# Performance work log

Measured on AMD Instinct MI355X. Metric: run time of the kernel, lower is better.

The kernel has to match this reference:

```python
import jax, jax.numpy as jnp
import numpy as np

S = 7          # side
B = 2          # boxes per cell
C = 20         # classes
L = S * S      # grid cells
NOOBJ = 0.5 * 1.0
OBJ   = 0.5 * 1.0
CLS   = 0.5 * 1.0
COORD = 0.5 * 5.0


def setup_inputs() -> dict:
    key = jax.random.key(0)
    k1, k2, k3 = jax.random.split(key, 3)
    n = 16384
    preds = jax.random.uniform(k1, (n, L * (C + 5 * B)), dtype=jnp.float32)
    labels = jax.random.uniform(k2, (n, L * (1 + C + 4)), dtype=jnp.float32)
    lab = labels.reshape(n, L, 1 + C + 4)
    obj_flag = (jax.random.uniform(k3, (n, L)) < 0.15).astype(jnp.float32)
    lab = lab.at[:, :, 0].set(obj_flag)
    labels = lab.reshape(n, -1)
    return {"preds": preds, "labels": labels}


def _iou(t, o):
    # t, o: [..., 4] boxes in (cx, cy, w, h); returns [...]
    left   = jnp.maximum(t[..., 0] - 0.5 * t[..., 2], o[..., 0] - 0.5 * o[..., 2])
    right  = jnp.minimum(t[..., 0] + 0.5 * t[..., 2], o[..., 0] + 0.5 * o[..., 2])
    top    = jnp.maximum(t[..., 1] - 0.5 * t[..., 3], o[..., 1] - 0.5 * o[..., 3])
    bottom = jnp.minimum(t[..., 1] + 0.5 * t[..., 3], o[..., 1] + 0.5 * o[..., 3])
    w = right - left
    h = bottom - top
    invalid = (w < 0) | (h < 0)
    inter = jnp.where(invalid, 0.0, w * h)
    union = t[..., 2] * t[..., 3] + o[..., 2] * o[..., 3] - inter
    return jnp.where(invalid, 0.0, inter / jnp.maximum(union, 1e-12))


def reference(preds, labels):
    n = preds.shape[0]
    pcls  = preds[:, : L * C].reshape(n, L, C)                       # [n,L,C]
    pconf = preds[:, L * C : L * C + L * B].reshape(n, L, B)          # [n,L,B]
    pbox  = preds[:, L * C + L * B :].reshape(n, L, B, 4)             # [n,L,B,4]

    lab  = labels.reshape(n, L, 1 + C + 4)
    obj  = lab[:, :, 0] != 0                                          # [n,L]
    tcls = lab[:, :, 1 : 1 + C]                                       # [n,L,C]
    tbox = lab[:, :, 1 + C :]                                         # [n,L,4] raw

    # --- best-box selection (on detached predictions, like .detach() in torch) ---
    o_raw = jax.lax.stop_gradient(pbox)
    o = jnp.concatenate([o_raw[..., :2] / S, o_raw[..., 2:] ** 2], axis=-1)      # [n,L,B,4]
    t = jnp.concatenate([tbox[..., :2] / S, tbox[..., 2:]], axis=-1)[:, :, None] # [n,L,1,4]
    t = jax.lax.stop_gradient(t)

    iou  = _iou(t, o)                                                 # [n,L,B]
    rmse = jnp.sqrt(jnp.sum((t - o) ** 2, axis=-1))                   # [n,L,B]
    max_iou = jnp.max(iou, axis=-1)
    # if any IoU>0 pick first argmax of IoU, else first argmin of RMSE (best_rmse init 20)
    best = jnp.where(max_iou > 0, jnp.argmax(iou, axis=-1), jnp.argmin(rmse, axis=-1))  # [n,L]
    best_iou = jnp.take_along_axis(iou, best[:, :, None], axis=-1)[..., 0]        # [n,L]

    onehot = jnp.arange(B) == best[:, :, None]                        # [n,L,B]
    mask_best = obj[:, :, None] & onehot

    # confidence delta: noobject everywhere, overwritten at best box of object cells
    conf_delta = jnp.where(mask_best,
                           OBJ * (best_iou[:, :, None] - pconf) ** 2,
                           NOOBJ * pconf ** 2)

    # class delta (object cells only)
    cls_delta = jnp.where(obj[:, :, None], CLS * (tcls - pcls) ** 2, 0.0)

    # coord delta at best box: raw truth x,y and sqrt(truth w,h) vs raw preds
    pbest = jnp.take_along_axis(pbox, best[:, :, None, None], axis=2)[:, :, 0]    # [n,L,4]
    ttarget = jnp.concatenate([tbox[..., :2], jnp.sqrt(tbox[..., 2:])], axis=-1)  # [n,L,4]
    coord_delta = jnp.where(obj[:, :, None], COORD * (ttarget - pbest) ** 2, 0.0)

    return jnp.nansum(conf_delta) + jnp.nansum(cls_delta) + jnp.nansum(coord_delta)
```

## Files before the change

kernel.cpp:

```cpp
#include <hip/hip_runtime.h>


#define L_CELLS 49
#define PRED_ROW 1470
#define LAB_ROW 1225
#define CONF_BASE 980
#define BOX_BASE 1078
#define W_NOOBJ 0.5f
#define W_OBJ 0.5f
#define W_CLS 0.5f
#define W_COORD 2.5f
#define INV_S (1.0f / 7.0f)

__global__ void zero_out_kernel(float* out) { out[0] = 0.0f; }

__global__ __launch_bounds__(256) void yolo_loss_kernel(
    const float* __restrict__ preds, const float* __restrict__ labels,
    float* __restrict__ out, int n) {
  int cell = blockIdx.x * blockDim.x + threadIdx.x;
  int total = n * L_CELLS;
  float acc = 0.0f;
  if (cell < total) {
    int sample = cell / L_CELLS;
    int l = cell - sample * L_CELLS;
    const float* rp = preds + (size_t)sample * PRED_ROW;
    const float* labc = labels + (size_t)sample * LAB_ROW + l * 25;

    float objf = labc[0];
    const float* confp = rp + CONF_BASE + l * 2;
    float c0 = confp[0];
    float c1 = confp[1];

    if (objf != 0.0f) {
      const float* boxp = rp + BOX_BASE + l * 8;
      float bx[8];
#pragma unroll
      for (int k = 0; k < 8; ++k) bx[k] = boxp[k];

      float tx = labc[21], ty = labc[22], tw = labc[23], th = labc[24];
      float t0 = tx * INV_S, t1 = ty * INV_S, t2 = tw, t3 = th;

      float iou[2], rmse2[2];
#pragma unroll
      for (int b = 0; b < 2; ++b) {
        float o0 = bx[4 * b + 0] * INV_S;
        float o1 = bx[4 * b + 1] * INV_S;
        float o2 = bx[4 * b + 2] * bx[4 * b + 2];
        float o3 = bx[4 * b + 3] * bx[4 * b + 3];
        float left = fmaxf(t0 - 0.5f * t2, o0 - 0.5f * o2);
        float right = fminf(t0 + 0.5f * t2, o0 + 0.5f * o2);
        float top = fmaxf(t1 - 0.5f * t3, o1 - 0.5f * o3);
        float bot = fminf(t1 + 0.5f * t3, o1 + 0.5f * o3);
        float w = right - left;
        float h = bot - top;
        bool invalid = (w < 0.0f) || (h < 0.0f);
        float inter = invalid ? 0.0f : w * h;
        float uni = t2 * t3 + o2 * o3 - inter;
        iou[b] = invalid ? 0.0f : inter / fmaxf(uni, 1e-12f);
        float d0 = t0 - o0, d1 = t1 - o1, d2 = t2 - o2, d3 = t3 - o3;
        rmse2[b] = d0 * d0 + d1 * d1 + d2 * d2 + d3 * d3;
      }

      float max_iou = fmaxf(iou[0], iou[1]);
      int best;
      if (max_iou > 0.0f)
        best = (iou[1] > iou[0]) ? 1 : 0;
      else
        best = (rmse2[1] < rmse2[0]) ? 1 : 0;
      float best_iou = iou[best];

      float cb = (best == 0) ? c0 : c1;
      float co = (best == 0) ? c1 : c0;
      float db = best_iou - cb;
      acc += W_OBJ * db * db + W_NOOBJ * co * co;

      const float* pcls = rp + l * 20;
      float clsacc = 0.0f;
#pragma unroll
      for (int c = 0; c < 20; ++c) {
        float d = labc[1 + c] - pcls[c];
        clsacc += d * d;
      }
      acc += W_CLS * clsacc;

      float e0 = tx - bx[best * 4 + 0];
      float e1 = ty - bx[best * 4 + 1];
      float e2 = sqrtf(tw) - bx[best * 4 + 2];
      float e3 = sqrtf(th) - bx[best * 4 + 3];
      acc += W_COORD * (e0 * e0 + e1 * e1 + e2 * e2 + e3 * e3);
    } else {
      acc = W_NOOBJ * (c0 * c0 + c1 * c1);
    }
  }

#pragma unroll
  for (int off = 32; off > 0; off >>= 1) acc += __shfl_down(acc, off);

  __shared__ float wsum[4];
  int wave = threadIdx.x >> 6;
  int lane = threadIdx.x & 63;
  if (lane == 0) wsum[wave] = acc;
  __syncthreads();
  if (threadIdx.x == 0) {
    float s = wsum[0] + wsum[1] + wsum[2] + wsum[3];
    atomicAdd(out, s);
  }
}

extern "C" void kernel_launch(void* const* d_in, const int* in_sizes, int n_in,
                              void* d_out, int out_size, void* d_ws, size_t ws_size,
                              hipStream_t stream) {
  const float* preds = (const float*)d_in[0];
  const float* labels = (const float*)d_in[1];
  float* out = (float*)d_out;
  int n = in_sizes[0] / PRED_ROW;
  int total = n * L_CELLS;
  int blocks = (total + 255) / 256;

  zero_out_kernel<<<1, 1, 0, stream>>>(out);
  yolo_loss_kernel<<<blocks, 256, 0, stream>>>(preds, labels, out, n);
}
```

Measured before the change: 203.0 us.

## Stage per-sample rows in shared memory with coalesced float4 loads

Switches from one thread per grid cell to one block per sample. The block cooperatively loads the full prediction and label rows into LDS with aligned float4 loads, then spreads the class-loss terms across all threads and computes the box/confidence terms with 49 threads. This replaces strided, uncoalesced per-thread global reads with coalesced streaming. In exchange it reads class data for empty cells too, and it issues more blocks, which means more atomics on the single output.

```diff
diff --git a/kernel.cpp b/kernel.cpp
--- a/kernel.cpp
+++ b/kernel.cpp
@@ -1,7 +1,6 @@
 #include <hip/hip_runtime.h>
 
 
-#define L_CELLS 49
 #define PRED_ROW 1470
 #define LAB_ROW 1225
 #define CONF_BASE 980
@@ -17,27 +16,77 @@
 __global__ __launch_bounds__(256) void yolo_loss_kernel(
     const float* __restrict__ preds, const float* __restrict__ labels,
     float* __restrict__ out, int n) {
-  int cell = blockIdx.x * blockDim.x + threadIdx.x;
-  int total = n * L_CELLS;
+  __shared__ float4 lab4[308];
+  __shared__ float4 pred4[368];
+
+  const int s = blockIdx.x;
+  const int tid = threadIdx.x;
+
+  size_t lrow = (size_t)s * LAB_ROW;
+  size_t lstart = lrow & ~(size_t)3;
+  int loff = (int)(lrow - lstart);
+  int ln4 = (loff + LAB_ROW + 3) >> 2;
+  size_t ltotal = (size_t)n * LAB_ROW;
+  for (int i = tid; i < ln4; i += 256) {
+    size_t g = lstart + 4 * (size_t)i;
+    float4 v;
+    if (g + 4 <= ltotal) {
+      v = *(const float4*)(labels + g);
+    } else {
+      v.x = (g + 0 < ltotal) ? labels[g + 0] : 0.0f;
+      v.y = (g + 1 < ltotal) ? labels[g + 1] : 0.0f;
+      v.z = (g + 2 < ltotal) ? labels[g + 2] : 0.0f;
+      v.w = (g + 3 < ltotal) ? labels[g + 3] : 0.0f;
+    }
+    lab4[i] = v;
+  }
+
+  size_t prow = (size_t)s * PRED_ROW;
+  size_t pstart = prow & ~(size_t)3;
+  int poff = (int)(prow - pstart);
+  int pn4 = (poff + PRED_ROW + 3) >> 2;
+  size_t ptotal = (size_t)n * PRED_ROW;
+  for (int i = tid; i < pn4; i += 256) {
+    size_t g = pstart + 4 * (size_t)i;
+    float4 v;
+    if (g + 4 <= ptotal) {
+      v = *(const float4*)(preds + g);
+    } else {
+      v.x = (g + 0 < ptotal) ? preds[g + 0] : 0.0f;
+      v.y = (g + 1 < ptotal) ? preds[g + 1] : 0.0f;
+      v.z = (g + 2 < ptotal) ? preds[g + 2] : 0.0f;
+      v.w = (g + 3 < ptotal) ? preds[g + 3] : 0.0f;
+    }
+    pred4[i] = v;
+  }
+
+  __syncthreads();
+
+  const float* lab = (const float*)lab4 + loff;
+  const float* pr = (const float*)pred4 + poff;
+
   float acc = 0.0f;
-  if (cell < total) {
-    int sample = cell / L_CELLS;
-    int l = cell - sample * L_CELLS;
-    const float* rp = preds + (size_t)sample * PRED_ROW;
-    const float* labc = labels + (size_t)sample * LAB_ROW + l * 25;
 
-    float objf = labc[0];
-    const float* confp = rp + CONF_BASE + l * 2;
-    float c0 = confp[0];
-    float c1 = confp[1];
+  for (int idx = tid; idx < CONF_BASE; idx += 256) {
+    int l = idx / 20;
+    int c = idx - l * 20;
+    if (lab[l * 25] != 0.0f) {
+      float d = lab[l * 25 + 1 + c] - pr[idx];
+      acc += W_CLS * d * d;
+    }
+  }
 
+  if (tid < 49) {
+    int l = tid;
+    float objf = lab[l * 25];
+    float c0 = pr[CONF_BASE + 2 * l];
+    float c1 = pr[CONF_BASE + 2 * l + 1];
     if (objf != 0.0f) {
-      const float* boxp = rp + BOX_BASE + l * 8;
       float bx[8];
 #pragma unroll
-      for (int k = 0; k < 8; ++k) bx[k] = boxp[k];
-
-      float tx = labc[21], ty = labc[22], tw = labc[23], th = labc[24];
+      for (int k = 0; k < 8; ++k) bx[k] = pr[BOX_BASE + 8 * l + k];
+      float tx = lab[l * 25 + 21], ty = lab[l * 25 + 22];
+      float tw = lab[l * 25 + 23], th = lab[l * 25 + 24];
       float t0 = tx * INV_S, t1 = ty * INV_S, t2 = tw, t3 = th;
 
       float iou[2], rmse2[2];
@@ -74,22 +123,13 @@
       float db = best_iou - cb;
       acc += W_OBJ * db * db + W_NOOBJ * co * co;
 
-      const float* pcls = rp + l * 20;
-      float clsacc = 0.0f;
-#pragma unroll
-      for (int c = 0; c < 20; ++c) {
-        float d = labc[1 + c] - pcls[c];
-        clsacc += d * d;
-      }
-      acc += W_CLS * clsacc;
-
       float e0 = tx - bx[best * 4 + 0];
       float e1 = ty - bx[best * 4 + 1];
       float e2 = sqrtf(tw) - bx[best * 4 + 2];
       float e3 = sqrtf(th) - bx[best * 4 + 3];
       acc += W_COORD * (e0 * e0 + e1 * e1 + e2 * e2 + e3 * e3);
     } else {
-      acc = W_NOOBJ * (c0 * c0 + c1 * c1);
+      acc += W_NOOBJ * (c0 * c0 + c1 * c1);
     }
   }
 
@@ -97,13 +137,12 @@
   for (int off = 32; off > 0; off >>= 1) acc += __shfl_down(acc, off);
 
   __shared__ float wsum[4];
-  int wave = threadIdx.x >> 6;
-  int lane = threadIdx.x & 63;
+  int wave = tid >> 6;
+  int lane = tid & 63;
   if (lane == 0) wsum[wave] = acc;
   __syncthreads();
-  if (threadIdx.x == 0) {
-    float s = wsum[0] + wsum[1] + wsum[2] + wsum[3];
-    atomicAdd(out, s);
+  if (tid == 0) {
+    atomicAdd(out, wsum[0] + wsum[1] + wsum[2] + wsum[3]);
   }
 }
 
@@ -114,9 +153,7 @@
   const float* labels = (const float*)d_in[1];
   float* out = (float*)d_out;
   int n = in_sizes[0] / PRED_ROW;
-  int total = n * L_CELLS;
-  int blocks = (total + 255) / 256;
 
   zero_out_kernel<<<1, 1, 0, stream>>>(out);
-  yolo_loss_kernel<<<blocks, 256, 0, stream>>>(preds, labels, out, n);
+  yolo_loss_kernel<<<n, 256, 0, stream>>>(preds, labels, out, n);
 }
```

Result: slower. 353.6 us (+74.2%).
